# Optimization experiments

Measured on AMD Instinct MI355X. Metric: run time of the kernel, lower is better.

Reference implementation:

```python
import jax, jax.numpy as jnp
import numpy as np

N_NODES = 15000
N_EDGES = 60000
D_NODE_IN = 74
D_EDGE_IN = 12
D = 64            # node_out_feats
D_EHID = 128      # edge_hidden_feats
N_STEPS = 6
BN_EPS = 1e-5


def setup_inputs() -> dict:
    key = jax.random.key(0)
    ks = jax.random.split(key, 16)
    def lin(k, fan_in, shape):
        return jax.random.normal(k, shape, jnp.float32) / np.sqrt(fan_in)
    inp = {
        "node_feats": jax.random.normal(ks[0], (N_NODES, D_NODE_IN), jnp.float32),
        "edge_feats": jax.random.normal(ks[1], (N_EDGES, D_EDGE_IN), jnp.float32),
        "src": jax.random.randint(ks[2], (N_EDGES,), 0, N_NODES, jnp.int32),
        "dst": jax.random.randint(ks[3], (N_EDGES,), 0, N_NODES, jnp.int32),
        # project_node_feats: Linear(node_in, D)
        "W_proj": lin(ks[4], D_NODE_IN, (D_NODE_IN, D)),
        "b_proj": jnp.zeros((D,), jnp.float32),
        # edge network: Linear(edge_in, ehid) -> ReLU -> Linear(ehid, D*D)
        "W_e1": lin(ks[5], D_EDGE_IN, (D_EDGE_IN, D_EHID)),
        "b_e1": jnp.zeros((D_EHID,), jnp.float32),
        "W_e2": lin(ks[6], D_EHID, (D_EHID, D * D)),
        "b_e2": jnp.zeros((D * D,), jnp.float32),
        # NNConv bias + BatchNorm affine params
        "conv_bias": jnp.zeros((D,), jnp.float32),
        "bn_gamma": jnp.ones((D,), jnp.float32),
        "bn_beta": jnp.zeros((D,), jnp.float32),
        # GRU (single layer): torch layout W_ih [3D, D], W_hh [3D, D]
        "W_ih": lin(ks[7], D, (3 * D, D)),
        "W_hh": lin(ks[8], D, (3 * D, D)),
        "b_ih": jnp.zeros((3 * D,), jnp.float32),
        "b_hh": jnp.zeros((3 * D,), jnp.float32),
    }
    return inp


def reference(node_feats, edge_feats, W_proj, b_proj, W_e1, b_e1, W_e2, b_e2,
              conv_bias, bn_gamma, bn_beta, W_ih, W_hh, b_ih, b_hh, src, dst):
    n_nodes = node_feats.shape[0]

    # project_node_feats: Linear + ReLU
    h = jax.nn.relu(node_feats @ W_proj + b_proj)          # [N, D]
    hidden = h                                              # GRU hidden state

    # edge MLP is a pure function of static edge_feats -> compute once
    ew = jax.nn.relu(edge_feats @ W_e1 + b_e1) @ W_e2 + b_e2
    ew = ew.reshape(-1, D, D)                               # [E, D, D]

    # mean-aggregation normalizer (DGL mean: 0 for isolated nodes)
    deg = jax.ops.segment_sum(jnp.ones_like(dst, jnp.float32), dst,
                              num_segments=n_nodes)
    inv_deg = jnp.where(deg > 0, 1.0 / jnp.maximum(deg, 1.0), 0.0)[:, None]

    for _ in range(N_STEPS):
        # per-edge matvec message: (h_src^T W_e); sum over d_in commutes
        # with the mean reduction, so reduce vectors instead of matrices.
        msg = jnp.einsum('ei,eio->eo', h[src], ew)          # [E, D]
        rst = jax.ops.segment_sum(msg, dst, num_segments=n_nodes) * inv_deg
        rst = rst + conv_bias
        # BatchNorm1d (training mode: batch statistics, biased variance)
        mu = rst.mean(axis=0)
        var = rst.var(axis=0)
        rst = (rst - mu) * jax.lax.rsqrt(var + BN_EPS) * bn_gamma + bn_beta
        m = jax.nn.relu(rst)
        # GRU cell (torch gate order: r, z, n)
        gi = m @ W_ih.T + b_ih
        gh = hidden @ W_hh.T + b_hh
        i_r, i_z, i_n = jnp.split(gi, 3, axis=-1)
        h_r, h_z, h_n = jnp.split(gh, 3, axis=-1)
        r = jax.nn.sigmoid(i_r + h_r)
        z = jax.nn.sigmoid(i_z + h_z)
        n = jnp.tanh(i_n + r * h_n)
        hidden = (1.0 - z) * n + z * hidden
        h = hidden
    return h
```

## Files before the change

kernel.cpp:

```cpp
#include <hip/hip_runtime.h>
#include <math.h>

#define NN 15000
#define NE 60000
#define DIN 74
#define DEIN 12
#define DD 64
#define EH 128
#define NG 8192
#define NSTEPS 6
#define NBN 59
#define KAB 384
#define NTMAX 18752
#define NFB 586

typedef unsigned short ushort_t;
typedef __attribute__((ext_vector_type(8))) short short8v;
typedef __attribute__((ext_vector_type(4))) float float4v;

__device__ __forceinline__ float bsf(unsigned short u){
  union { unsigned int i; float f; } v; v.i = ((unsigned int)u) << 16; return v.f;
}
__device__ __forceinline__ unsigned short fsb(float f){
  union { float f; unsigned int i; } v; v.f = f;
  unsigned int x = v.i;
  return (unsigned short)((x + 0x7FFFu + ((x >> 16) & 1u)) >> 16);
}

__global__ void k_sniff(const ushort_t* __restrict__ nf16,
                        const int* __restrict__ dsti, int* __restrict__ flags){
  __shared__ int cnt[2];
  int t = threadIdx.x;
  if (t < 2) cnt[t] = 0;
  __syncthreads();
  int bad = 0;
  for (int i = t; i < 1024; i += 256){
    unsigned short u = nf16[2*i];
    int e = (u >> 7) & 0xFF;
    if (e < 96 || e > 159) bad++;
  }
  if (bad) atomicAdd(&cnt[0], bad);
  if (t < 256 && dsti[2*t+1] == 0) atomicAdd(&cnt[1], 1);
  __syncthreads();
  if (t == 0){
    flags[0] = (cnt[0] > 300) ? 1 : 0;
    flags[1] = (cnt[1] > 250) ? 1 : 0;
  }
}

struct CanonArgs {
  const void* in[15];
  float* out[15];
  int n[15];
};
__global__ void k_canon_all(CanonArgs a, const int* __restrict__ flags){
  int j = blockIdx.y;
  int n = a.n[j];
  int fp32 = flags[0];
  const void* in = a.in[j];
  float* out = a.out[j];
  for (int i = blockIdx.x*256 + threadIdx.x; i < n; i += gridDim.x*256){
    if (fp32) out[i] = ((const float*)in)[i];
    else      out[i] = bsf(((const ushort_t*)in)[i]);
  }
}
__global__ void k_canoni(const void* __restrict__ in, int* __restrict__ out,
                         int n, const int* __restrict__ flags){
  int i = blockIdx.x*256 + threadIdx.x;
  if (i >= n) return;
  long long v = flags[1] ? ((const long long*)in)[i]
                         : (long long)((const int*)in)[i];
  int vi = (int)v;
  if (vi < 0) vi = 0;
  if (vi >= NN) vi = NN-1;
  out[i] = vi;
}

__global__ void k_proj(const float* __restrict__ nf, const float* __restrict__ Wp,
                       const float* __restrict__ bp, float* __restrict__ hid,
                       ushort_t* __restrict__ ab){
  __shared__ float nfl[4][DIN];
  int t = threadIdx.x, blk = blockIdx.x;
  for (int idx = t; idx < 4*DIN; idx += 256){
    int vl = idx / DIN, i = idx - vl*DIN;
    nfl[vl][i] = nf[(size_t)(blk*4+vl)*DIN + i];
  }
  __syncthreads();
  int vl = t >> 6, o = t & 63;
  int v = blk*4 + vl;
  float acc = bp[o];
  for (int i = 0; i < DIN; ++i) acc += nfl[vl][i] * Wp[i*DD + o];
  float r = fmaxf(acc, 0.f);
  hid[(size_t)v*DD + o] = r;
  ushort_t hh = fsb(r);
  float hl = r - bsf(hh);
  ab[(size_t)v*KAB + 64 + o]  = hh;
  ab[(size_t)v*KAB + 192 + o] = fsb(hl);
  ab[(size_t)v*KAB + 320 + o] = hh;
}

__global__ void k_emlp(const float* __restrict__ ef, const float* __restrict__ W1,
                       const float* __restrict__ b1, ushort_t* __restrict__ thi,
                       ushort_t* __restrict__ tlo){
  __shared__ float efl[2][DEIN];
  int t = threadIdx.x, blk = blockIdx.x;
  if (t < 2*DEIN){
    int el = t / DEIN, i = t - el*DEIN;
    efl[el][i] = ef[(size_t)(blk*2+el)*DEIN + i];
  }
  __syncthreads();
  int el = t >> 7, c = t & 127;
  float acc = b1[c];
  for (int i = 0; i < DEIN; ++i) acc += efl[el][i] * W1[i*EH + c];
  float tv = fmaxf(acc, 0.f);
  ushort_t hiv = fsb(tv);
  size_t off = (size_t)(blk*2+el)*EH + c;
  thi[off] = hiv;
  tlo[off] = fsb(tv - bsf(hiv));
}
__global__ void k_zpad(ushort_t* __restrict__ thi, ushort_t* __restrict__ tlo){
  int t = threadIdx.x;
  thi[(size_t)NE*EH + t] = 0;
  tlo[(size_t)NE*EH + t] = 0;
}

__global__ void k_w2q(const float* __restrict__ W2, const float* __restrict__ b2,
                      ushort_t* __restrict__ w2q, ushort_t* __restrict__ w2b){
  int idx = blockIdx.x*256 + threadIdx.x;
  if (idx < NG*DD){
    int n = idx >> 6, i = idx & 63;
    int kq = n >> 11, rem = n & 2047;
    int o = rem >> 5, kl = rem & 31;
    int kg = kq*32 + kl;
    w2q[idx] = fsb(W2[(size_t)kg*4096 + i*64 + o]);
  } else if (idx < NG*DD + DD*DD){
    int r = idx - NG*DD;
    int o = r >> 6, i = r & 63;
    w2b[r] = fsb(b2[i*64 + o]);
  }
}

__global__ void k_wgru(const float* __restrict__ Wih, const float* __restrict__ Whh,
                       ushort_t* __restrict__ wg){
  int pos = blockIdx.x*256 + threadIdx.x;
  if (pos >= 256*KAB) return;
  int c = pos / KAB, k = pos - c*KAB;
  int kb = k >> 6, i = k & 63;
  int g = c >> 6, o = c & 63;
  float w = 0.f;
  if ((kb & 1) == 0){
    if (g == 0)      w = Wih[(size_t)(o)*64 + i];
    else if (g == 1) w = Wih[(size_t)(64+o)*64 + i];
    else if (g == 2) w = Wih[(size_t)(128+o)*64 + i];
  } else {
    if (g == 0)      w = Whh[(size_t)(o)*64 + i];
    else if (g == 1) w = Whh[(size_t)(64+o)*64 + i];
    else if (g == 3) w = Whh[(size_t)(128+o)*64 + i];
  }
  ushort_t hi = fsb(w);
  wg[pos] = (kb >= 4) ? fsb(w - bsf(hi)) : hi;
}

__global__ void k_zero(int* __restrict__ p, int n){
  int i = blockIdx.x*256 + threadIdx.x;
  if (i < n) p[i] = 0;
}
__global__ void k_deg(const int* __restrict__ idxarr, int* __restrict__ deg){
  int e = blockIdx.x*256 + threadIdx.x;
  if (e < NE) atomicAdd(&deg[idxarr[e]], 1);
}
__global__ void k_invd(const int* __restrict__ deg, float* __restrict__ invd){
  int i = blockIdx.x*256 + threadIdx.x;
  if (i < NN){
    int d = deg[i];
    invd[i] = (d > 0) ? 1.0f/(float)d : 0.0f;
  }
}
__global__ void k_scan(const int* __restrict__ deg, int* __restrict__ rowp,
                       float* __restrict__ invd){
  __shared__ int ssum[256];
  int t = threadIdx.x;
  const int STRIP = (NN + 255) / 256;
  int lo = t*STRIP, hi = (lo + STRIP < NN) ? lo + STRIP : NN;
  int s = 0;
  for (int i = lo; i < hi; ++i) s += deg[i];
  ssum[t] = s;
  __syncthreads();
  if (t == 0){
    int acc = 0;
    for (int i = 0; i < 256; ++i){ int v = ssum[i]; ssum[i] = acc; acc += v; }
  }
  __syncthreads();
  int acc = ssum[t];
  for (int i = lo; i < hi; ++i){
    rowp[i] = acc;
    int d = deg[i];
    invd[i] = (d > 0) ? 1.0f/(float)d : 0.0f;
    acc += d;
  }
  if (t == 255) rowp[NN] = acc;
}
__global__ void k_scatter(const int* __restrict__ idxarr, const int* __restrict__ rowp,
                          int* __restrict__ cursor, int* __restrict__ eidx){
  int e = blockIdx.x*256 + threadIdx.x;
  if (e < NE){
    int d = idxarr[e];
    int pos = atomicAdd(&cursor[d], 1);
    eidx[rowp[d] + pos] = e;
  }
}

__global__ void k_tiles(const int* __restrict__ rowp, int* __restrict__ tnode,
                        int* __restrict__ tbase, int* __restrict__ tcnt,
                        int* __restrict__ ntb){
  __shared__ int ss[256];
  int t = threadIdx.x;
  const int STRIP = (NN + 255) / 256;
  int lo = t*STRIP, hi = lo + STRIP; if (hi > NN) hi = NN;
  int c = 0;
  for (int i = lo; i < hi; ++i){
    int deg = rowp[i+1] - rowp[i];
    c += (deg + 15) >> 4;
  }
  ss[t] = c;
  __syncthreads();
  if (t == 0){
    int a = 0;
    for (int i = 0; i < 256; ++i){ int v = ss[i]; ss[i] = a; a += v; }
    ntb[0] = a;
  }
  __syncthreads();
  int pos = ss[t];
  for (int i = lo; i < hi; ++i){
    int b = rowp[i], deg = rowp[i+1] - b;
    for (int r = 0; r < deg; r += 16){
      tnode[pos] = i; tbase[pos] = b + r;
      int c2 = deg - r; tcnt[pos] = (c2 > 16) ? 16 : c2;
      ++pos;
    }
  }
}

__global__ void k_rstinit(const float* __restrict__ cbias, float* __restrict__ rst){
  int i = blockIdx.x*256 + threadIdx.x;
  if (i < NN*DD) rst[i] = cbias[i & 63];
}

__global__ __launch_bounds__(512,4) void k_fused2(
    const ushort_t* __restrict__ ab, const ushort_t* __restrict__ w2q,
    const ushort_t* __restrict__ w2b, const ushort_t* __restrict__ thi,
    const ushort_t* __restrict__ tlo,
    const int* __restrict__ tnode, const int* __restrict__ tbase,
    const int* __restrict__ tcnt, const int* __restrict__ ntb,
    const int* __restrict__ eidx, const int* __restrict__ dstc,
    const float* __restrict__ invd, float* __restrict__ rst){
  __shared__ __align__(16) ushort_t Gl[32768];
  __shared__ float bhl[32*66];
  __shared__ int nodl[32], cntl[32], basel[32];
  __shared__ int eidl[32][16];
  __shared__ int dstl[32][16];

  int tid = threadIdx.x;
  int nt = ntb[0];
  int T0 = blockIdx.x * 32;
  if (T0 >= nt) return;
  int wv = tid >> 6, lane = tid & 63;
  int lr = lane & 15, quad = lane >> 4;

  if (tid < 32){
    int gt = T0 + tid;
    int node = 0, base = 0, cnt = 0;
    if (gt < nt){ node = tnode[gt]; base = tbase[gt]; cnt = tcnt[gt]; }
    nodl[tid] = node; basel[tid] = base; cntl[tid] = cnt;
  }
  __syncthreads();
  {
    int j = tid >> 4, sl = tid & 15;
    int eid = NE, d = -1;
    if (sl < cntl[j]){
      eid = eidx[basel[j] + sl];
      d = dstc[eid];
    }
    eidl[j][sl] = eid;
    dstl[j][sl] = d;
  }
  short8v hf0k0, hf0k1, hf1k0, hf1k1;
  {
    int n0 = nodl[lr], n1 = nodl[16 + lr];
    hf0k0 = *(const short8v*)(ab + (size_t)n0*KAB + 64 + quad*8);
    hf0k1 = *(const short8v*)(ab + (size_t)n0*KAB + 96 + quad*8);
    hf1k0 = *(const short8v*)(ab + (size_t)n1*KAB + 64 + quad*8);
    hf1k1 = *(const short8v*)(ab + (size_t)n1*KAB + 96 + quad*8);
  }
  {
    int ot = wv & 3, mh = wv >> 2;
    float4v ba = (float4v){0.f,0.f,0.f,0.f};
    short8v a0 = *(const short8v*)(w2b + (size_t)(ot*16 + lr)*DD + quad*8);
    short8v a1 = *(const short8v*)(w2b + (size_t)(ot*16 + lr)*DD + 32 + quad*8);
    ba = __builtin_amdgcn_mfma_f32_16x16x32_bf16(a0, mh ? hf1k0 : hf0k0, ba, 0,0,0);
    ba = __builtin_amdgcn_mfma_f32_16x16x32_bf16(a1, mh ? hf1k1 : hf0k1, ba, 0,0,0);
    #pragma unroll
    for (int reg = 0; reg < 4; ++reg)
      bhl[(mh*16 + lr)*66 + ot*16 + quad*4 + reg] = ba[reg];
  }

  int j0 = wv*4;
  for (int oh = 0; oh < 2; ++oh){
    float4v acc[4][2];
    #pragma unroll
    for (int j = 0; j < 4; ++j)
      #pragma unroll
      for (int ot = 0; ot < 2; ++ot)
        acc[j][ot] = (float4v){0.f,0.f,0.f,0.f};
    for (int kq = 0; kq < 4; ++kq){
      __syncthreads();
      #pragma unroll 2
      for (int it = 0; it < 8; ++it){
        int tile = wv*8 + it;
        int nrow = kq*2048 + oh*1024 + tile*16 + lr;
        const ushort_t* arow = w2q + (size_t)nrow*DD;
        short8v a0 = *(const short8v*)(arow + quad*8);
        short8v a1 = *(const short8v*)(arow + 32 + quad*8);
        int ol = tile >> 1;
        int klb = ((tile & 1) << 4) + quad*4;
        int q8 = klb >> 3, jj = klb & 7;
        #pragma unroll
        for (int mh = 0; mh < 2; ++mh){
          float4v g = (float4v){0.f,0.f,0.f,0.f};
          g = __builtin_amdgcn_mfma_f32_16x16x32_bf16(a0, mh ? hf1k0 : hf0k0, g, 0,0,0);
          g = __builtin_amdgcn_mfma_f32_16x16x32_bf16(a1, mh ? hf1k1 : hf0k1, g, 0,0,0);
          int m = mh*16 + lr;
          unsigned int p0 = (unsigned int)fsb(g[0]) | ((unsigned int)fsb(g[1]) << 16);
          unsigned int p1 = (unsigned int)fsb(g[2]) | ((unsigned int)fsb(g[3]) << 16);
          int byt = ((((m*4 + q8)*32 + ol) << 4) + jj*2) ^ ((m & 7) << 4);
          uint2 pv; pv.x = p0; pv.y = p1;
          *(uint2*)((char*)Gl + byt) = pv;
        }
      }
      __syncthreads();
      short8v th0, th1, th2, th3, tw0, tw1, tw2, tw3;
      {
        size_t kqo = (size_t)kq*32 + quad*8;
        int e0 = eidl[j0+0][lr], e1 = eidl[j0+1][lr];
        int e2 = eidl[j0+2][lr], e3 = eidl[j0+3][lr];
        th0 = *(const short8v*)(thi + (size_t)e0*EH + kqo);
        tw0 = *(const short8v*)(tlo + (size_t)e0*EH + kqo);
        th1 = *(const short8v*)(thi + (size_t)e1*EH + kqo);
        tw1 = *(const short8v*)(tlo + (size_t)e1*EH + kqo);
        th2 = *(const short8v*)(thi + (size_t)e2*EH + kqo);
        tw2 = *(const short8v*)(tlo + (size_t)e2*EH + kqo);
        th3 = *(const short8v*)(thi + (size_t)e3*EH + kqo);
        tw3 = *(const short8v*)(tlo + (size_t)e3*EH + kqo);
      }
      #pragma unroll
      for (int j = 0; j < 4; ++j){
        int m = j0 + j;
        int swz = (m & 7) << 4;
        short8v thj = (j==0)?th0:(j==1)?th1:(j==2)?th2:th3;
        short8v twj = (j==0)?tw0:(j==1)?tw1:(j==2)?tw2:tw3;
        #pragma unroll
        for (int ot = 0; ot < 2; ++ot){
          int byt = (((m*4 + quad)*32 + ot*16 + lr) << 4) ^ swz;
          short8v gf = *(const short8v*)((const char*)Gl + byt);
          acc[j][ot] = __builtin_amdgcn_mfma_f32_16x16x32_bf16(thj, gf, acc[j][ot], 0,0,0);
          acc[j][ot] = __builtin_amdgcn_mfma_f32_16x16x32_bf16(twj, gf, acc[j][ot], 0,0,0);
        }
      }
    }
    #pragma unroll
    for (int j = 0; j < 4; ++j){
      int m = j0 + j;
      #pragma unroll
      for (int ot = 0; ot < 2; ++ot){
        int o = oh*32 + ot*16 + lr;
        float bb = bhl[m*66 + o];
        #pragma unroll
        for (int reg = 0; reg < 4; ++reg){
          int d = dstl[m][quad*4 + reg];
          if (d >= 0)
            atomicAdd(&rst[(size_t)d*DD + o], (acc[j][ot][reg] + bb) * invd[d]);
        }
      }
    }
  }
}

__global__ void k_bnp(const float* __restrict__ rst, float* __restrict__ part){
  __shared__ float ls[256], ls2[256];
  int t = threadIdx.x, blk = blockIdx.x;
  int o = t & 63, gg = t >> 6;
  int r0 = blk*256;
  float s = 0.f, s2 = 0.f;
  for (int j = 0; j < 64; ++j){
    int r = r0 + gg + j*4;
    if (r < NN){
      float x = rst[(size_t)r*DD + o];
      s += x; s2 += x*x;
    }
  }
  ls[t] = s; ls2[t] = s2;
  __syncthreads();
  if (gg == 0){
    part[blk*128 + o]      = ls[o] + ls[64+o] + ls[128+o] + ls[192+o];
    part[blk*128 + 64 + o] = ls2[o] + ls2[64+o] + ls2[128+o] + ls2[192+o];
  }
}
__global__ void k_bnf(const float* __restrict__ part, float* __restrict__ stats){
  __shared__ float sh[128];
  int t = threadIdx.x;
  float s = 0.f;
  for (int b = 0; b < NBN; ++b) s += part[b*128 + t];
  sh[t] = s;
  __syncthreads();
  if (t < 64){
    float mu = sh[t] / (float)NN;
    float var = sh[64+t] / (float)NN - mu*mu;
    if (var < 0.f) var = 0.f;
    stats[t] = mu;
    stats[64 + t] = rsqrtf(var + 1e-5f);
  }
}

__global__ void k_gru_pre(const float* __restrict__ rst, const float* __restrict__ stats,
      const float* __restrict__ gamma, const float* __restrict__ beta,
      const float* __restrict__ cbias,
      ushort_t* __restrict__ ab, float* __restrict__ rstw){
  int t = threadIdx.x, blk = blockIdx.x;
  int vl = t >> 6, o = t & 63;
  int v = blk*4 + vl;
  float x = rst[(size_t)v*DD + o];
  float m = fmaxf((x - stats[o])*stats[64+o]*gamma[o] + beta[o], 0.f);
  ushort_t mh = fsb(m);
  float mlo = m - bsf(mh);
  ab[(size_t)v*KAB + o]       = mh;
  ab[(size_t)v*KAB + 128 + o] = fsb(mlo);
  ab[(size_t)v*KAB + 256 + o] = mh;
  rstw[(size_t)v*DD + o] = cbias[o];
}

__global__ __launch_bounds__(256) void k_gru_gemm(const ushort_t* __restrict__ ab,
        const ushort_t* __restrict__ wg, float* __restrict__ gbuf){
  __shared__ __align__(16) ushort_t As[128][136];
  __shared__ __align__(16) ushort_t Bs[64][136];
  int t = threadIdx.x;
  int n0 = blockIdx.x * 64;
  int m0 = blockIdx.y * 128;
  int w = t >> 6, lane = t & 63;
  int lrow = lane & 15, quad = lane >> 4;
  float4v acc[2][4];
  #pragma unroll
  for (int mt = 0; mt < 2; ++mt)
    #pragma unroll
    for (int nt = 0; nt < 4; ++nt) acc[mt][nt] = (float4v){0.f,0.f,0.f,0.f};
  for (int kt = 0; kt < 3; ++kt){
    __syncthreads();
    #pragma unroll
    for (int it = 0; it < 8; ++it){
      int cid = t + it*256;
      int r = cid >> 4, ko = (cid & 15) * 8;
      int gm = m0 + r; if (gm >= NN) gm = NN-1;
      *(uint4*)&As[r][ko] = *(const uint4*)(ab + (size_t)gm*KAB + kt*128 + ko);
    }
    #pragma unroll
    for (int it = 0; it < 4; ++it){
      int cid = t + it*256;
      int r = cid >> 4, ko = (cid & 15) * 8;
      *(uint4*)&Bs[r][ko] = *(const uint4*)(wg + (size_t)(n0 + r)*KAB + kt*128 + ko);
    }
    __syncthreads();
    #pragma unroll
    for (int ks = 0; ks < 4; ++ks){
      short8v a0 = *(const short8v*)&As[w*32 + lrow][ks*32 + quad*8];
      short8v a1 = *(const short8v*)&As[w*32 + 16 + lrow][ks*32 + quad*8];
      #pragma unroll
      for (int nt = 0; nt < 4; ++nt){
        short8v b = *(const short8v*)&Bs[nt*16 + lrow][ks*32 + quad*8];
        acc[0][nt] = __builtin_amdgcn_mfma_f32_16x16x32_bf16(a0, b, acc[0][nt], 0, 0, 0);
        acc[1][nt] = __builtin_amdgcn_mfma_f32_16x16x32_bf16(a1, b, acc[1][nt], 0, 0, 0);
      }
    }
  }
  #pragma unroll
  for (int mt = 0; mt < 2; ++mt){
    #pragma unroll
    for (int nt = 0; nt < 4; ++nt){
      int col = n0 + nt*16 + lrow;
      #pragma unroll
      for (int reg = 0; reg < 4; ++reg){
        int m = m0 + w*32 + mt*16 + quad*4 + reg;
        if (m < NN) gbuf[(size_t)m*256 + col] = acc[mt][nt][reg];
      }
    }
  }
}

__global__ void k_gru_fin(const float* __restrict__ gbuf,
      const float* __restrict__ bih, const float* __restrict__ bhh,
      float* __restrict__ hid, ushort_t* __restrict__ ab,
      float* __restrict__ out, int write_out){
  int t = threadIdx.x, blk = blockIdx.x;
  int vl = t >> 6, o = t & 63;
  int v = blk*4 + vl;
  const float* gb = gbuf + (size_t)v*256;
  float aR  = gb[o]       + bih[o]      + bhh[o];
  float aZ  = gb[64 + o]  + bih[64+o]   + bhh[64+o];
  float aNi = gb[128 + o] + bih[128+o];
  float aNh = gb[192 + o] + bhh[128+o];
  float hprev = hid[(size_t)v*DD + o];
  float r = 1.f/(1.f+__expf(-aR));
  float z = 1.f/(1.f+__expf(-aZ));
  float n = tanhf(aNi + r*aNh);
  float hnew = (1.f - z)*n + z*hprev;
  hid[(size_t)v*DD + o] = hnew;
  ushort_t hh = fsb(hnew);
  float hl = hnew - bsf(hh);
  ab[(size_t)v*KAB + 64 + o]  = hh;
  ab[(size_t)v*KAB + 192 + o] = fsb(hl);
  ab[(size_t)v*KAB + 320 + o] = hh;
  if (write_out) out[(size_t)v*DD + o] = hnew;
}

extern "C" void kernel_launch(void* const* d_in, const int* in_sizes, int n_in,
                              void* d_out, int out_size, void* d_ws, size_t ws_size,
                              hipStream_t stream){
  (void)out_size; (void)ws_size;
  float* out = (float*)d_out;

  int p_nf=-1,p_ef=-1,p_src=-1,p_dst=-1,p_Wp=-1,p_bp=-1,p_W1=-1,p_b1=-1,
      p_W2=-1,p_b2=-1,p_cb=-1,p_gam=-1,p_bet=-1,p_Wih=-1,p_Whh=-1,p_bih=-1,p_bhh=-1;
  int c60000=0,c64=0,c12288=0,c192=0;
  for (int i = 0; i < n_in; ++i){
    switch (in_sizes[i]){
      case 1110000: p_nf = i; break;
      case 720000:  p_ef = i; break;
      case 60000:   if (c60000++ == 0) p_src = i; else p_dst = i; break;
      case 4736:    p_Wp = i; break;
      case 64:      { if (c64==0) p_bp=i; else if (c64==1) p_cb=i;
                      else if (c64==2) p_gam=i; else p_bet=i; c64++; } break;
      case 1536:    p_W1 = i; break;
      case 128:     p_b1 = i; break;
      case 524288:  p_W2 = i; break;
      case 4096:    p_b2 = i; break;
      case 12288:   if (c12288++ == 0) p_Wih = i; else p_Whh = i; break;
      case 192:     if (c192++ == 0) p_bih = i; else p_bhh = i; break;
      default: break;
    }
  }

  char* p = (char*)d_ws;
  auto alloc = [&](size_t bytes)->char*{
    char* r = p; p += (bytes + 255) & ~(size_t)255; return r;
  };
  int* flags = (int*)alloc(256);
  const int FPOS[15] = {p_nf,p_ef,p_Wp,p_bp,p_W1,p_b1,p_W2,p_b2,p_cb,p_gam,p_bet,
                        p_Wih,p_Whh,p_bih,p_bhh};
  CanonArgs ca;
  int maxn = 0;
  for (int j = 0; j < 15; ++j){
    int n = in_sizes[FPOS[j]];
    ca.in[j]  = d_in[FPOS[j]];
    ca.out[j] = (float*)alloc((size_t)n * 4);
    ca.n[j]   = n;
    if (n > maxn) maxn = n;
  }
  const float* nf  = ca.out[0];  const float* ef  = ca.out[1];
  const float* Wp  = ca.out[2];  const float* bp  = ca.out[3];
  const float* W1  = ca.out[4];  const float* b1  = ca.out[5];
  const float* W2  = ca.out[6];  const float* b2  = ca.out[7];
  const float* cb  = ca.out[8];  const float* gam = ca.out[9];
  const float* bet = ca.out[10]; const float* Wih = ca.out[11];
  const float* Whh = ca.out[12]; const float* bih = ca.out[13];
  const float* bhh = ca.out[14];
  int* srcc = (int*)alloc((size_t)NE*4);
  int* dstc = (int*)alloc((size_t)NE*4);

  ushort_t* thi   = (ushort_t*)alloc((size_t)(NE+1)*EH*2);
  ushort_t* tlo   = (ushort_t*)alloc((size_t)(NE+1)*EH*2);
  ushort_t* w2q   = (ushort_t*)alloc((size_t)NG*DD*2);
  ushort_t* w2b   = (ushort_t*)alloc((size_t)DD*DD*2);
  float* hid      = (float*)alloc((size_t)NN*DD*4);
  ushort_t* ab    = (ushort_t*)alloc((size_t)NN*KAB*2);
  ushort_t* wg    = (ushort_t*)alloc((size_t)256*KAB*2);
  float* gbuf     = (float*)alloc((size_t)NN*256*4);
  float* rst      = (float*)alloc((size_t)NN*DD*4);
  float* part     = (float*)alloc((size_t)NBN*128*4);
  float* stats    = (float*)alloc(128*4);
  int* degall     = (int*)alloc((size_t)4*NN*4);
  int* deg  = degall;
  int* deg2 = degall + 2*NN; int* cursor2 = degall + 3*NN;
  float* invd = (float*)alloc((size_t)NN*4);
  int* rowp2  = (int*)alloc((size_t)(NN+1)*4);
  float* invd2= (float*)alloc((size_t)NN*4);
  int* eidx2  = (int*)alloc((size_t)NE*4);
  int* tnode  = (int*)alloc((size_t)NTMAX*4);
  int* tbase  = (int*)alloc((size_t)NTMAX*4);
  int* tcnt   = (int*)alloc((size_t)NTMAX*4);
  int* ntb    = (int*)alloc(256);

  k_sniff<<<1, 256, 0, stream>>>((const ushort_t*)d_in[p_nf], (const int*)d_in[p_dst], flags);
  k_canon_all<<<dim3((maxn+255)/256, 15), 256, 0, stream>>>(ca, flags);
  k_canoni<<<(NE+255)/256, 256, 0, stream>>>(d_in[p_src], srcc, NE, flags);
  k_canoni<<<(NE+255)/256, 256, 0, stream>>>(d_in[p_dst], dstc, NE, flags);

  k_proj <<<NN/4,  256, 0, stream>>>(nf, Wp, bp, hid, ab);
  k_emlp <<<NE/2,  256, 0, stream>>>(ef, W1, b1, thi, tlo);
  k_zpad <<<1, 128, 0, stream>>>(thi, tlo);
  k_w2q  <<<(NG*DD + DD*DD + 255)/256, 256, 0, stream>>>(W2, b2, w2q, w2b);
  k_wgru <<<(256*KAB+255)/256, 256, 0, stream>>>(Wih, Whh, wg);
  k_zero <<<(4*NN+255)/256, 256, 0, stream>>>(degall, 4*NN);
  k_deg  <<<(NE+255)/256, 256, 0, stream>>>(dstc, deg);
  k_deg  <<<(NE+255)/256, 256, 0, stream>>>(srcc, deg2);
  k_invd <<<(NN+255)/256, 256, 0, stream>>>(deg, invd);
  k_scan <<<1, 256, 0, stream>>>(deg2, rowp2, invd2);
  k_scatter<<<(NE+255)/256, 256, 0, stream>>>(srcc, rowp2, cursor2, eidx2);
  k_tiles<<<1, 256, 0, stream>>>(rowp2, tnode, tbase, tcnt, ntb);
  k_rstinit<<<(NN*DD+255)/256, 256, 0, stream>>>(cb, rst);

  for (int s = 0; s < NSTEPS; ++s){
    k_fused2<<<NFB, 512, 0, stream>>>(ab, w2q, w2b, thi, tlo,
                                      tnode, tbase, tcnt, ntb,
                                      eidx2, dstc, invd, rst);
    k_bnp <<<NBN, 256, 0, stream>>>(rst, part);
    k_bnf <<<1, 128, 0, stream>>>(part, stats);
    k_gru_pre <<<NN/4, 256, 0, stream>>>(rst, stats, gam, bet, cb, ab, rst);
    k_gru_gemm<<<dim3(4, (NN+127)/128), 256, 0, stream>>>(ab, wg, gbuf);
    k_gru_fin <<<NN/4, 256, 0, stream>>>(gbuf, bih, bhh, hid, ab, out,
                                         (s == NSTEPS-1) ? 1 : 0);
  }
}
```

Baseline: 1.136 ms.

## Prefetch W2 tiles in registers, merge output halves, fold BN finalize into GRU pre

The fused message kernel now keeps all four output groups' accumulators live and interleaves the two output halves inside the k-loop. Edge-feature loads are issued once per k-chunk and the next W2 tile is register-prefetched while the current LDS tile is consumed. This hides global load latency and avoids reloading edge features per half, but it raises register pressure, so launch bounds drop to 2 blocks. Separately, the single-block BN finalize kernel is removed and each k_gru_pre block reduces the partial sums itself, which saves one launch per step at the cost of redundant reductions.

Result: slower. 1.307 ms (+15.1%).

```diff
diff --git a/kernel.cpp b/kernel.cpp
--- a/kernel.cpp
+++ b/kernel.cpp
@@ -246,7 +246,7 @@
   if (i < NN*DD) rst[i] = cbias[i & 63];
 }
 
-__global__ __launch_bounds__(512,4) void k_fused2(
+__global__ __launch_bounds__(512,2) void k_fused4(
     const ushort_t* __restrict__ ab, const ushort_t* __restrict__ w2q,
     const ushort_t* __restrict__ w2b, const ushort_t* __restrict__ thi,
     const ushort_t* __restrict__ tlo,
@@ -284,51 +284,70 @@
     eidl[j][sl] = eid;
     dstl[j][sl] = d;
   }
-  short8v hf0k0, hf0k1, hf1k0, hf1k1;
+  __syncthreads();
+  int j0 = wv*4;
+  int ej[4];
+  #pragma unroll
+  for (int j = 0; j < 4; ++j) ej[j] = eidl[j0+j][lr];
+
+  short8v hf[2][2];
   {
     int n0 = nodl[lr], n1 = nodl[16 + lr];
-    hf0k0 = *(const short8v*)(ab + (size_t)n0*KAB + 64 + quad*8);
-    hf0k1 = *(const short8v*)(ab + (size_t)n0*KAB + 96 + quad*8);
-    hf1k0 = *(const short8v*)(ab + (size_t)n1*KAB + 64 + quad*8);
-    hf1k1 = *(const short8v*)(ab + (size_t)n1*KAB + 96 + quad*8);
+    hf[0][0] = *(const short8v*)(ab + (size_t)n0*KAB + 64 + quad*8);
+    hf[0][1] = *(const short8v*)(ab + (size_t)n0*KAB + 96 + quad*8);
+    hf[1][0] = *(const short8v*)(ab + (size_t)n1*KAB + 64 + quad*8);
+    hf[1][1] = *(const short8v*)(ab + (size_t)n1*KAB + 96 + quad*8);
   }
   {
     int ot = wv & 3, mh = wv >> 2;
     float4v ba = (float4v){0.f,0.f,0.f,0.f};
     short8v a0 = *(const short8v*)(w2b + (size_t)(ot*16 + lr)*DD + quad*8);
     short8v a1 = *(const short8v*)(w2b + (size_t)(ot*16 + lr)*DD + 32 + quad*8);
-    ba = __builtin_amdgcn_mfma_f32_16x16x32_bf16(a0, mh ? hf1k0 : hf0k0, ba, 0,0,0);
-    ba = __builtin_amdgcn_mfma_f32_16x16x32_bf16(a1, mh ? hf1k1 : hf0k1, ba, 0,0,0);
+    ba = __builtin_amdgcn_mfma_f32_16x16x32_bf16(a0, hf[mh][0], ba, 0,0,0);
+    ba = __builtin_amdgcn_mfma_f32_16x16x32_bf16(a1, hf[mh][1], ba, 0,0,0);
     #pragma unroll
     for (int reg = 0; reg < 4; ++reg)
       bhl[(mh*16 + lr)*66 + ot*16 + quad*4 + reg] = ba[reg];
   }
 
-  int j0 = wv*4;
-  for (int oh = 0; oh < 2; ++oh){
-    float4v acc[4][2];
-    #pragma unroll
-    for (int j = 0; j < 4; ++j)
+  float4v acc[4][4];
+  #pragma unroll
+  for (int j = 0; j < 4; ++j)
+    #pragma unroll
+    for (int og = 0; og < 4; ++og)
+      acc[j][og] = (float4v){0.f,0.f,0.f,0.f};
+
+  short8v A0[8], A1[8];
+  #pragma unroll
+  for (int it = 0; it < 8; ++it){
+    int nrow = (wv*8 + it)*16 + lr;
+    A0[it] = *(const short8v*)(w2q + (size_t)nrow*DD + quad*8);
+    A1[it] = *(const short8v*)(w2q + (size_t)nrow*DD + 32 + quad*8);
+  }
+
+  short8v th[4], tw[4];
+  for (int kq = 0; kq < 4; ++kq){
+    #pragma unroll
+    for (int oh = 0; oh < 2; ++oh){
+      __syncthreads();
+      if (oh == 0){
+        #pragma unroll
+        for (int j = 0; j < 4; ++j){
+          th[j] = *(const short8v*)(thi + (size_t)ej[j]*EH + kq*32 + quad*8);
+          tw[j] = *(const short8v*)(tlo + (size_t)ej[j]*EH + kq*32 + quad*8);
+        }
+      }
       #pragma unroll
-      for (int ot = 0; ot < 2; ++ot)
-        acc[j][ot] = (float4v){0.f,0.f,0.f,0.f};
-    for (int kq = 0; kq < 4; ++kq){
-      __syncthreads();
-      #pragma unroll 2
       for (int it = 0; it < 8; ++it){
         int tile = wv*8 + it;
-        int nrow = kq*2048 + oh*1024 + tile*16 + lr;
-        const ushort_t* arow = w2q + (size_t)nrow*DD;
-        short8v a0 = *(const short8v*)(arow + quad*8);
-        short8v a1 = *(const short8v*)(arow + 32 + quad*8);
         int ol = tile >> 1;
         int klb = ((tile & 1) << 4) + quad*4;
         int q8 = klb >> 3, jj = klb & 7;
         #pragma unroll
         for (int mh = 0; mh < 2; ++mh){
           float4v g = (float4v){0.f,0.f,0.f,0.f};
-          g = __builtin_amdgcn_mfma_f32_16x16x32_bf16(a0, mh ? hf1k0 : hf0k0, g, 0,0,0);
-          g = __builtin_amdgcn_mfma_f32_16x16x32_bf16(a1, mh ? hf1k1 : hf0k1, g, 0,0,0);
+          g = __builtin_amdgcn_mfma_f32_16x16x32_bf16(A0[it], hf[mh][0], g, 0,0,0);
+          g = __builtin_amdgcn_mfma_f32_16x16x32_bf16(A1[it], hf[mh][1], g, 0,0,0);
           int m = mh*16 + lr;
           unsigned int p0 = (unsigned int)fsb(g[0]) | ((unsigned int)fsb(g[1]) << 16);
           unsigned int p1 = (unsigned int)fsb(g[2]) | ((unsigned int)fsb(g[3]) << 16);
@@ -337,49 +356,45 @@
           *(uint2*)((char*)Gl + byt) = pv;
         }
       }
+      {
+        int kqn, ohn;
+        if (oh == 0){ kqn = kq; ohn = 1; }
+        else { kqn = (kq < 3) ? kq + 1 : 3; ohn = 0; }
+        int rb = kqn*2048 + ohn*1024;
+        #pragma unroll
+        for (int it = 0; it < 8; ++it){
+          int nrow = rb + (wv*8 + it)*16 + lr;
+          A0[it] = *(const short8v*)(w2q + (size_t)nrow*DD + quad*8);
+          A1[it] = *(const short8v*)(w2q + (size_t)nrow*DD + 32 + quad*8);
+        }
+      }
       __syncthreads();
-      short8v th0, th1, th2, th3, tw0, tw1, tw2, tw3;
-      {
-        size_t kqo = (size_t)kq*32 + quad*8;
-        int e0 = eidl[j0+0][lr], e1 = eidl[j0+1][lr];
-        int e2 = eidl[j0+2][lr], e3 = eidl[j0+3][lr];
-        th0 = *(const short8v*)(thi + (size_t)e0*EH + kqo);
-        tw0 = *(const short8v*)(tlo + (size_t)e0*EH + kqo);
-        th1 = *(const short8v*)(thi + (size_t)e1*EH + kqo);
-        tw1 = *(const short8v*)(tlo + (size_t)e1*EH + kqo);
-        th2 = *(const short8v*)(thi + (size_t)e2*EH + kqo);
-        tw2 = *(const short8v*)(tlo + (size_t)e2*EH + kqo);
-        th3 = *(const short8v*)(thi + (size_t)e3*EH + kqo);
-        tw3 = *(const short8v*)(tlo + (size_t)e3*EH + kqo);
-      }
       #pragma unroll
       for (int j = 0; j < 4; ++j){
         int m = j0 + j;
         int swz = (m & 7) << 4;
-        short8v thj = (j==0)?th0:(j==1)?th1:(j==2)?th2:th3;
-        short8v twj = (j==0)?tw0:(j==1)?tw1:(j==2)?tw2:tw3;
         #pragma unroll
         for (int ot = 0; ot < 2; ++ot){
           int byt = (((m*4 + quad)*32 + ot*16 + lr) << 4) ^ swz;
           short8v gf = *(const short8v*)((const char*)Gl + byt);
-          acc[j][ot] = __builtin_amdgcn_mfma_f32_16x16x32_bf16(thj, gf, acc[j][ot], 0,0,0);
-          acc[j][ot] = __builtin_amdgcn_mfma_f32_16x16x32_bf16(twj, gf, acc[j][ot], 0,0,0);
+          acc[j][oh*2+ot] = __builtin_amdgcn_mfma_f32_16x16x32_bf16(th[j], gf, acc[j][oh*2+ot], 0,0,0);
+          acc[j][oh*2+ot] = __builtin_amdgcn_mfma_f32_16x16x32_bf16(tw[j], gf, acc[j][oh*2+ot], 0,0,0);
         }
       }
     }
-    #pragma unroll
-    for (int j = 0; j < 4; ++j){
-      int m = j0 + j;
+  }
+  #pragma unroll
+  for (int j = 0; j < 4; ++j){
+    int m = j0 + j;
+    #pragma unroll
+    for (int og = 0; og < 4; ++og){
+      int o = og*16 + lr;
+      float bb = bhl[m*66 + o];
       #pragma unroll
-      for (int ot = 0; ot < 2; ++ot){
-        int o = oh*32 + ot*16 + lr;
-        float bb = bhl[m*66 + o];
-        #pragma unroll
-        for (int reg = 0; reg < 4; ++reg){
-          int d = dstl[m][quad*4 + reg];
-          if (d >= 0)
-            atomicAdd(&rst[(size_t)d*DD + o], (acc[j][ot][reg] + bb) * invd[d]);
-        }
+      for (int reg = 0; reg < 4; ++reg){
+        int d = dstl[m][quad*4 + reg];
+        if (d >= 0)
+          atomicAdd(&rst[(size_t)d*DD + o], (acc[j][og][reg] + bb) * invd[d]);
       }
     }
   }
@@ -405,31 +420,27 @@
     part[blk*128 + 64 + o] = ls2[o] + ls2[64+o] + ls2[128+o] + ls2[192+o];
   }
 }
-__global__ void k_bnf(const float* __restrict__ part, float* __restrict__ stats){
-  __shared__ float sh[128];
-  int t = threadIdx.x;
-  float s = 0.f;
-  for (int b = 0; b < NBN; ++b) s += part[b*128 + t];
-  sh[t] = s;
-  __syncthreads();
-  if (t < 64){
-    float mu = sh[t] / (float)NN;
-    float var = sh[64+t] / (float)NN - mu*mu;
-    if (var < 0.f) var = 0.f;
-    stats[t] = mu;
-    stats[64 + t] = rsqrtf(var + 1e-5f);
-  }
-}
-
-__global__ void k_gru_pre(const float* __restrict__ rst, const float* __restrict__ stats,
+
+__global__ void k_gru_pre(const float* __restrict__ rst, const float* __restrict__ part,
       const float* __restrict__ gamma, const float* __restrict__ beta,
       const float* __restrict__ cbias,
       ushort_t* __restrict__ ab, float* __restrict__ rstw){
+  __shared__ float st[128];
   int t = threadIdx.x, blk = blockIdx.x;
+  if (t < 128){
+    float s = 0.f;
+    for (int b = 0; b < NBN; ++b) s += part[b*128 + t];
+    st[t] = s;
+  }
+  __syncthreads();
   int vl = t >> 6, o = t & 63;
   int v = blk*4 + vl;
+  float mu = st[o] / (float)NN;
+  float var = st[64+o] / (float)NN - mu*mu;
+  if (var < 0.f) var = 0.f;
+  float rs = rsqrtf(var + 1e-5f);
   float x = rst[(size_t)v*DD + o];
-  float m = fmaxf((x - stats[o])*stats[64+o]*gamma[o] + beta[o], 0.f);
+  float m = fmaxf((x - mu)*rs*gamma[o] + beta[o], 0.f);
   ushort_t mh = fsb(m);
   float mlo = m - bsf(mh);
   ab[(size_t)v*KAB + o]       = mh;
@@ -584,7 +595,6 @@
   float* gbuf     = (float*)alloc((size_t)NN*256*4);
   float* rst      = (float*)alloc((size_t)NN*DD*4);
   float* part     = (float*)alloc((size_t)NBN*128*4);
-  float* stats    = (float*)alloc(128*4);
   int* degall     = (int*)alloc((size_t)4*NN*4);
   int* deg  = degall;
   int* deg2 = degall + 2*NN; int* cursor2 = degall + 3*NN;
@@ -617,12 +627,11 @@
   k_rstinit<<<(NN*DD+255)/256, 256, 0, stream>>>(cb, rst);
 
   for (int s = 0; s < NSTEPS; ++s){
-    k_fused2<<<NFB, 512, 0, stream>>>(ab, w2q, w2b, thi, tlo,
+    k_fused4<<<NFB, 512, 0, stream>>>(ab, w2q, w2b, thi, tlo,
                                       tnode, tbase, tcnt, ntb,
                                       eidx2, dstc, invd, rst);
     k_bnp <<<NBN, 256, 0, stream>>>(rst, part);
-    k_bnf <<<1, 128, 0, stream>>>(part, stats);
-    k_gru_pre <<<NN/4, 256, 0, stream>>>(rst, stats, gam, bet, cb, ab, rst);
+    k_gru_pre <<<NN/4, 256, 0, stream>>>(rst, part, gam, bet, cb, ab, rst);
     k_gru_gemm<<<dim3(4, (NN+127)/128), 256, 0, stream>>>(ab, wg, gbuf);
     k_gru_fin <<<NN/4, 256, 0, stream>>>(gbuf, bih, bhh, hid, ab, out,
                                          (s == NSTEPS-1) ? 1 : 0);
```

## Replace atomic scatter of messages with CSR-by-destination gather reduction fused with BN stats

Applied to the files above, without the earlier changes.

The message kernel now writes each per-edge message to a dense [E,64] buffer instead of atomically adding into per-node rows. A new reduction kernel walks a destination-sorted CSR (built once at setup) to sum messages per node, applies the inverse degree and conv bias, and accumulates the BatchNorm partial sums in the same pass. This removes the float atomics and the per-step rst re-initialisation, at the cost of an extra ~15MB write and read of messages per step. The reduction result is also deterministic.

Result: no change. 1.129 ms (-0.6%).

```diff
diff --git a/kernel.cpp b/kernel.cpp
--- a/kernel.cpp
+++ b/kernel.cpp
@@ -9,7 +9,7 @@
 #define EH 128
 #define NG 8192
 #define NSTEPS 6
-#define NBN 59
+#define NRB 235
 #define KAB 384
 #define NTMAX 18752
 #define NFB 586
@@ -169,13 +169,6 @@
   int e = blockIdx.x*256 + threadIdx.x;
   if (e < NE) atomicAdd(&deg[idxarr[e]], 1);
 }
-__global__ void k_invd(const int* __restrict__ deg, float* __restrict__ invd){
-  int i = blockIdx.x*256 + threadIdx.x;
-  if (i < NN){
-    int d = deg[i];
-    invd[i] = (d > 0) ? 1.0f/(float)d : 0.0f;
-  }
-}
 __global__ void k_scan(const int* __restrict__ deg, int* __restrict__ rowp,
                        float* __restrict__ invd){
   __shared__ int ssum[256];
@@ -241,24 +234,17 @@
   }
 }
 
-__global__ void k_rstinit(const float* __restrict__ cbias, float* __restrict__ rst){
-  int i = blockIdx.x*256 + threadIdx.x;
-  if (i < NN*DD) rst[i] = cbias[i & 63];
-}
-
-__global__ __launch_bounds__(512,4) void k_fused2(
+__global__ __launch_bounds__(512,4) void k_fused5(
     const ushort_t* __restrict__ ab, const ushort_t* __restrict__ w2q,
     const ushort_t* __restrict__ w2b, const ushort_t* __restrict__ thi,
     const ushort_t* __restrict__ tlo,
     const int* __restrict__ tnode, const int* __restrict__ tbase,
     const int* __restrict__ tcnt, const int* __restrict__ ntb,
-    const int* __restrict__ eidx, const int* __restrict__ dstc,
-    const float* __restrict__ invd, float* __restrict__ rst){
+    const int* __restrict__ eidx, float* __restrict__ msg){
   __shared__ __align__(16) ushort_t Gl[32768];
   __shared__ float bhl[32*66];
   __shared__ int nodl[32], cntl[32], basel[32];
   __shared__ int eidl[32][16];
-  __shared__ int dstl[32][16];
 
   int tid = threadIdx.x;
   int nt = ntb[0];
@@ -276,13 +262,9 @@
   __syncthreads();
   {
     int j = tid >> 4, sl = tid & 15;
-    int eid = NE, d = -1;
-    if (sl < cntl[j]){
-      eid = eidx[basel[j] + sl];
-      d = dstc[eid];
-    }
+    int eid = NE;
+    if (sl < cntl[j]) eid = eidx[basel[j] + sl];
     eidl[j][sl] = eid;
-    dstl[j][sl] = d;
   }
   short8v hf0k0, hf0k1, hf1k0, hf1k1;
   {
@@ -376,27 +358,41 @@
         float bb = bhl[m*66 + o];
         #pragma unroll
         for (int reg = 0; reg < 4; ++reg){
-          int d = dstl[m][quad*4 + reg];
-          if (d >= 0)
-            atomicAdd(&rst[(size_t)d*DD + o], (acc[j][ot][reg] + bb) * invd[d]);
+          int eid = eidl[m][quad*4 + reg];
+          if (eid < NE) msg[(size_t)eid*DD + o] = acc[j][ot][reg] + bb;
         }
       }
     }
   }
 }
 
-__global__ void k_bnp(const float* __restrict__ rst, float* __restrict__ part){
+__global__ void k_red(const float* __restrict__ msg, const int* __restrict__ rowp_d,
+                      const int* __restrict__ eidx_d, const float* __restrict__ invd,
+                      const float* __restrict__ cbias, float* __restrict__ rst,
+                      float* __restrict__ part){
   __shared__ float ls[256], ls2[256];
   int t = threadIdx.x, blk = blockIdx.x;
   int o = t & 63, gg = t >> 6;
-  int r0 = blk*256;
+  float cb = cbias[o];
   float s = 0.f, s2 = 0.f;
-  for (int j = 0; j < 64; ++j){
-    int r = r0 + gg + j*4;
-    if (r < NN){
-      float x = rst[(size_t)r*DD + o];
-      s += x; s2 += x*x;
-    }
+  #pragma unroll 1
+  for (int j = 0; j < 16; ++j){
+    int n = blk*64 + gg*16 + j;
+    if (n >= NN) break;
+    int b = rowp_d[n], e = rowp_d[n+1];
+    float a0 = 0.f, a1 = 0.f, a2 = 0.f, a3 = 0.f;
+    int i = b;
+    for (; i + 3 < e; i += 4){
+      int e0 = eidx_d[i], e1 = eidx_d[i+1], e2 = eidx_d[i+2], e3 = eidx_d[i+3];
+      a0 += msg[(size_t)e0*DD + o];
+      a1 += msg[(size_t)e1*DD + o];
+      a2 += msg[(size_t)e2*DD + o];
+      a3 += msg[(size_t)e3*DD + o];
+    }
+    for (; i < e; ++i) a0 += msg[(size_t)eidx_d[i]*DD + o];
+    float x = ((a0 + a1) + (a2 + a3)) * invd[n] + cb;
+    rst[(size_t)n*DD + o] = x;
+    s += x; s2 += x*x;
   }
   ls[t] = s; ls2[t] = s2;
   __syncthreads();
@@ -405,12 +401,20 @@
     part[blk*128 + 64 + o] = ls2[o] + ls2[64+o] + ls2[128+o] + ls2[192+o];
   }
 }
+
 __global__ void k_bnf(const float* __restrict__ part, float* __restrict__ stats){
   __shared__ float sh[128];
   int t = threadIdx.x;
-  float s = 0.f;
-  for (int b = 0; b < NBN; ++b) s += part[b*128 + t];
-  sh[t] = s;
+  float s0 = 0.f, s1 = 0.f, s2 = 0.f, s3 = 0.f;
+  int b = 0;
+  for (; b + 3 < NRB; b += 4){
+    s0 += part[b*128 + t];
+    s1 += part[(b+1)*128 + t];
+    s2 += part[(b+2)*128 + t];
+    s3 += part[(b+3)*128 + t];
+  }
+  for (; b < NRB; ++b) s0 += part[b*128 + t];
+  sh[t] = (s0 + s1) + (s2 + s3);
   __syncthreads();
   if (t < 64){
     float mu = sh[t] / (float)NN;
@@ -423,8 +427,7 @@
 
 __global__ void k_gru_pre(const float* __restrict__ rst, const float* __restrict__ stats,
       const float* __restrict__ gamma, const float* __restrict__ beta,
-      const float* __restrict__ cbias,
-      ushort_t* __restrict__ ab, float* __restrict__ rstw){
+      ushort_t* __restrict__ ab){
   int t = threadIdx.x, blk = blockIdx.x;
   int vl = t >> 6, o = t & 63;
   int v = blk*4 + vl;
@@ -435,7 +438,6 @@
   ab[(size_t)v*KAB + o]       = mh;
   ab[(size_t)v*KAB + 128 + o] = fsb(mlo);
   ab[(size_t)v*KAB + 256 + o] = mh;
-  rstw[(size_t)v*DD + o] = cbias[o];
 }
 
 __global__ __launch_bounds__(256) void k_gru_gemm(const ushort_t* __restrict__ ab,
@@ -542,7 +544,7 @@
       case 524288:  p_W2 = i; break;
       case 4096:    p_b2 = i; break;
       case 12288:   if (c12288++ == 0) p_Wih = i; else p_Whh = i; break;
-      case 192:     if (c192++ == 0) p_bih = i; else p_bhh = i; break;
+      case 192:    if (c192++ == 0) p_bih = i; else p_bhh = i; break;
       default: break;
     }
   }
@@ -583,12 +585,16 @@
   ushort_t* wg    = (ushort_t*)alloc((size_t)256*KAB*2);
   float* gbuf     = (float*)alloc((size_t)NN*256*4);
   float* rst      = (float*)alloc((size_t)NN*DD*4);
-  float* part     = (float*)alloc((size_t)NBN*128*4);
+  float* msg      = (float*)alloc((size_t)NE*DD*4);
+  float* part     = (float*)alloc((size_t)NRB*128*4);
   float* stats    = (float*)alloc(128*4);
   int* degall     = (int*)alloc((size_t)4*NN*4);
   int* deg  = degall;
+  int* curd = degall + NN;
   int* deg2 = degall + 2*NN; int* cursor2 = degall + 3*NN;
   float* invd = (float*)alloc((size_t)NN*4);
+  int* rowp_d = (int*)alloc((size_t)(NN+1)*4);
+  int* eidx_d = (int*)alloc((size_t)NE*4);
   int* rowp2  = (int*)alloc((size_t)(NN+1)*4);
   float* invd2= (float*)alloc((size_t)NN*4);
   int* eidx2  = (int*)alloc((size_t)NE*4);
@@ -610,19 +616,18 @@
   k_zero <<<(4*NN+255)/256, 256, 0, stream>>>(degall, 4*NN);
   k_deg  <<<(NE+255)/256, 256, 0, stream>>>(dstc, deg);
   k_deg  <<<(NE+255)/256, 256, 0, stream>>>(srcc, deg2);
-  k_invd <<<(NN+255)/256, 256, 0, stream>>>(deg, invd);
+  k_scan <<<1, 256, 0, stream>>>(deg,  rowp_d, invd);
   k_scan <<<1, 256, 0, stream>>>(deg2, rowp2, invd2);
+  k_scatter<<<(NE+255)/256, 256, 0, stream>>>(dstc, rowp_d, curd, eidx_d);
   k_scatter<<<(NE+255)/256, 256, 0, stream>>>(srcc, rowp2, cursor2, eidx2);
   k_tiles<<<1, 256, 0, stream>>>(rowp2, tnode, tbase, tcnt, ntb);
-  k_rstinit<<<(NN*DD+255)/256, 256, 0, stream>>>(cb, rst);
 
   for (int s = 0; s < NSTEPS; ++s){
-    k_fused2<<<NFB, 512, 0, stream>>>(ab, w2q, w2b, thi, tlo,
-                                      tnode, tbase, tcnt, ntb,
-                                      eidx2, dstc, invd, rst);
-    k_bnp <<<NBN, 256, 0, stream>>>(rst, part);
+    k_fused5<<<NFB, 512, 0, stream>>>(ab, w2q, w2b, thi, tlo,
+                                      tnode, tbase, tcnt, ntb, eidx2, msg);
+    k_red <<<NRB, 256, 0, stream>>>(msg, rowp_d, eidx_d, invd, cb, rst, part);
     k_bnf <<<1, 128, 0, stream>>>(part, stats);
-    k_gru_pre <<<NN/4, 256, 0, stream>>>(rst, stats, gam, bet, cb, ab, rst);
+    k_gru_pre <<<NN/4, 256, 0, stream>>>(rst, stats, gam, bet, ab);
     k_gru_gemm<<<dim3(4, (NN+127)/128), 256, 0, stream>>>(ab, wg, gbuf);
     k_gru_fin <<<NN/4, 256, 0, stream>>>(gbuf, bih, bhh, hid, ab, out,
                                          (s == NSTEPS-1) ? 1 : 0);
```
